# Optimization experiments

Hardware: AMD Instinct MI355X
Metric: run time of the kernel (lower is better)

The kernel has to match this reference:

```python
import jax, jax.numpy as jnp
import numpy as np

OUT_SIZE = 7
SAMPLE_NUM = 2
FEATMAP_STRIDES = (4, 8, 16, 32)
FINEST_SCALE = 56.0
IMG_H, IMG_W = 800, 1216
NUM_ROIS = 1024


def _bilinear_gather(feat, b, ys, xs):
    """Bilinearly sample feat[b] at grid (ys x xs).
    feat: [B,C,H,W]; b: [K] int32; ys,xs: [K,S] float sample coords.
    Returns [K,S,S,C].
    """
    H, W = feat.shape[2], feat.shape[3]
    valid_y = (ys >= -1.0) & (ys <= H)
    valid_x = (xs >= -1.0) & (xs <= W)
    y = jnp.clip(ys, 0.0)
    x = jnp.clip(xs, 0.0)
    yl = jnp.floor(y).astype(jnp.int32)
    xl = jnp.floor(x).astype(jnp.int32)
    # edge handling as in the CUDA roi_align kernel
    y = jnp.where(yl >= H - 1, jnp.asarray(H - 1, y.dtype), y)
    x = jnp.where(xl >= W - 1, jnp.asarray(W - 1, x.dtype), x)
    yl = jnp.minimum(yl, H - 1)
    xl = jnp.minimum(xl, W - 1)
    yh = jnp.minimum(yl + 1, H - 1)
    xh = jnp.minimum(xl + 1, W - 1)
    ly = y - yl.astype(y.dtype)
    lx = x - xl.astype(x.dtype)
    hy = 1.0 - ly
    hx = 1.0 - lx
    bb = b[:, None, None]                      # [K,1,1]
    Yl, Yh = yl[:, :, None], yh[:, :, None]    # [K,S,1]
    Xl, Xh = xl[:, None, :], xh[:, None, :]    # [K,1,S]

    def g(yi, xi):
        return feat[bb, :, yi, xi]             # [K,S,S,C]

    w_ll = (hy[:, :, None] * hx[:, None, :])[..., None]
    w_lh = (hy[:, :, None] * lx[:, None, :])[..., None]
    w_hl = (ly[:, :, None] * hx[:, None, :])[..., None]
    w_hh = (ly[:, :, None] * lx[:, None, :])[..., None]
    out = g(Yl, Xl) * w_ll
    out = out + g(Yl, Xh) * w_lh
    out = out + g(Yh, Xl) * w_hl
    out = out + g(Yh, Xh) * w_hh
    valid = (valid_y[:, :, None] & valid_x[:, None, :])[..., None]
    return jnp.where(valid, out, 0.0)


def roi_align(feat, rois, spatial_scale, out_size=OUT_SIZE, sr=SAMPLE_NUM):
    """RoIAlign (aligned=False, mmdet-v1 style). feat [B,C,H,W], rois [K,5].
    Returns [K,C,out,out].
    """
    K = rois.shape[0]
    C = feat.shape[1]
    b = rois[:, 0].astype(jnp.int32)
    x1 = rois[:, 1] * spatial_scale
    y1 = rois[:, 2] * spatial_scale
    x2 = rois[:, 3] * spatial_scale
    y2 = rois[:, 4] * spatial_scale
    roi_w = jnp.maximum(x2 - x1, 1.0)
    roi_h = jnp.maximum(y2 - y1, 1.0)
    S = out_size * sr
    grid = jnp.arange(S, dtype=feat.dtype) + 0.5  # [S]
    ys = y1[:, None] + grid[None, :] * (roi_h / S)[:, None]  # [K,S]
    xs = x1[:, None] + grid[None, :] * (roi_w / S)[:, None]
    v = _bilinear_gather(feat, b, ys, xs)                    # [K,S,S,C]
    v = v.reshape(K, out_size, sr, out_size, sr, C).mean(axis=(2, 4))
    return jnp.transpose(v, (0, 3, 1, 2))                    # [K,C,out,out]


def setup_inputs() -> dict:
    key = jax.random.key(0)
    ks = jax.random.split(key, 10)
    shapes = [(2, 256, 200, 304), (2, 256, 100, 152), (2, 256, 50, 76), (2, 256, 25, 38)]
    feats = [jax.random.normal(ks[i], s, dtype=jnp.float32) for i, s in enumerate(shapes)]
    K = NUM_ROIS
    b = jax.random.randint(ks[4], (K,), 0, 2).astype(jnp.float32)
    cx = jax.random.uniform(ks[5], (K,)) * IMG_W
    cy = jax.random.uniform(ks[6], (K,)) * IMG_H
    # box sizes spanning 8..512 px so all 4 FPN levels are exercised
    w = 2.0 ** (jax.random.uniform(ks[7], (K,)) * 6.0 + 3.0)
    h = 2.0 ** (jax.random.uniform(ks[8], (K,)) * 6.0 + 3.0)
    x1 = jnp.clip(cx - w * 0.5, 0.0, IMG_W - 1.0)
    y1 = jnp.clip(cy - h * 0.5, 0.0, IMG_H - 1.0)
    x2 = jnp.clip(cx + w * 0.5, 0.0, IMG_W - 1.0)
    y2 = jnp.clip(cy + h * 0.5, 0.0, IMG_H - 1.0)
    x2 = jnp.maximum(x2, x1)
    y2 = jnp.maximum(y2, y1)
    rois = jnp.stack([b, x1, y1, x2, y2], axis=-1)
    return {"feat0": feats[0], "feat1": feats[1], "feat2": feats[2], "feat3": feats[3], "rois": rois}


def reference(feat0, feat1, feat2, feat3, rois):
    feats = [feat0, feat1, feat2, feat3]
    num_levels = len(feats)
    # map_roi_levels
    scale = jnp.sqrt((rois[:, 3] - rois[:, 1] + 1.0) * (rois[:, 4] - rois[:, 2] + 1.0))
    lvls = jnp.floor(jnp.log2(scale / FINEST_SCALE + 1e-6))
    lvls = jnp.clip(lvls, 0, num_levels - 1).astype(jnp.int32)
    out = jnp.zeros((rois.shape[0], feat0.shape[1], OUT_SIZE, OUT_SIZE), dtype=feat0.dtype)
    for i in range(num_levels):
        rf = roi_align(feats[i], rois, 1.0 / FEATMAP_STRIDES[i])
        out = jnp.where((lvls == i)[:, None, None, None], rf, out)
    return out
```

## Files before the change

kernel.cpp:

```cpp
#include <hip/hip_runtime.h>

typedef unsigned int uint32;

namespace {
constexpr int CCH = 256;
constexpr int OUT = 7;
constexpr int S   = 14;
constexpr int NUM_ROIS = 1024;

constexpr int H0 = 200, W0 = 304;
constexpr int H1 = 100, W1 = 152;
constexpr int H2 = 50,  W2 = 76;
constexpr int H3 = 25,  W3 = 38;

constexpr size_t US0 = (size_t)2 * H0 * W0 * CCH;
constexpr size_t US1 = (size_t)2 * H1 * W1 * CCH;
constexpr size_t US2 = (size_t)2 * H2 * W2 * CCH;
constexpr size_t US3 = (size_t)2 * H3 * W3 * CCH;

constexpr int T0 = 10 * H0 * 2;
constexpr int T1 = 5  * H1 * 2;
constexpr int T2 = 3  * H2 * 2;
constexpr int T3 = 2  * H3 * 2;
}

__device__ __forceinline__ unsigned short f2bf(float f) {
    uint32 u = __float_as_uint(f);
    u += 0x7fffu + ((u >> 16) & 1u);
    return (unsigned short)(u >> 16);
}
__device__ __forceinline__ float blo(uint32 u) { return __uint_as_float(u << 16); }
__device__ __forceinline__ float bhi(uint32 u) { return __uint_as_float(u & 0xffff0000u); }

__global__ __launch_bounds__(256) void transpose_bf16(
    const float* __restrict__ f0, const float* __restrict__ f1,
    const float* __restrict__ f2, const float* __restrict__ f3,
    unsigned short* __restrict__ o0, unsigned short* __restrict__ o1,
    unsigned short* __restrict__ o2, unsigned short* __restrict__ o3)
{
    __shared__ __align__(16) unsigned short lds[32 * 264];
    int r = blockIdx.x;
    const float* in; unsigned short* op; int H, W, TX;
    if (r < T0)           {            in = f0; op = o0; H = H0; W = W0; TX = 10; }
    else if (r < T0+T1)   { r -= T0;   in = f1; op = o1; H = H1; W = W1; TX = 5; }
    else if (r < T0+T1+T2){ r -= T0+T1; in = f2; op = o2; H = H2; W = W2; TX = 3; }
    else                  { r -= T0+T1+T2; in = f3; op = o3; H = H3; W = W3; TX = 2; }
    const int tx = r % TX; r /= TX;
    const int y = r % H;
    const int b = r / H;
    const int x0 = tx * 32;
    const int t = threadIdx.x;

    {
        const int xq = t & 7;
        const int c0 = t >> 3;
        const int x  = x0 + 4 * xq;
        const bool w4 = ((W & 3) == 0) && (x + 3 < W);
        #pragma unroll
        for (int i = 0; i < 8; ++i) {
            const int c = c0 + (i << 5);
            const float* src = in + (((size_t)(b * CCH + c) * H + y) * W + x);
            float4 v = make_float4(0.f, 0.f, 0.f, 0.f);
            if (w4) {
                v = *reinterpret_cast<const float4*>(src);
            } else {
                if (x     < W) v.x = src[0];
                if (x + 1 < W) v.y = src[1];
                if (x + 2 < W) v.z = src[2];
                if (x + 3 < W) v.w = src[3];
            }
            unsigned short* dst = &lds[(4 * xq) * 264 + c];
            dst[0 * 264] = f2bf(v.x);
            dst[1 * 264] = f2bf(v.y);
            dst[2 * 264] = f2bf(v.z);
            dst[3 * 264] = f2bf(v.w);
        }
    }
    __syncthreads();
    {
        const int cg  = t & 31;
        const int xr0 = t >> 5;
        #pragma unroll
        for (int i = 0; i < 4; ++i) {
            const int xr = xr0 + 8 * i;
            const int x  = x0 + xr;
            if (x < W) {
                uint4 v = *reinterpret_cast<const uint4*>(&lds[xr * 264 + 8 * cg]);
                *reinterpret_cast<uint4*>(
                    op + (((size_t)b * H + y) * W + x) * CCH + 8 * cg) = v;
            }
        }
    }
}

__global__ __launch_bounds__(256) void roi_gather_bf16(
    const unsigned short* __restrict__ w0, const unsigned short* __restrict__ w1,
    const unsigned short* __restrict__ w2, const unsigned short* __restrict__ w3,
    const float* __restrict__ rois, float* __restrict__ out)
{
    const int k = blockIdx.x;
    const int t = threadIdx.x;

    __shared__ float s_wlo[2][S];
    __shared__ float s_whi[2][S];
    __shared__ int   s_olo[2][S];
    __shared__ int   s_ohi[2][S];
    __shared__ __align__(16) float s_out[25 * 260];

    const float rb  = rois[k*5+0];
    const float rx1 = rois[k*5+1];
    const float ry1 = rois[k*5+2];
    const float rx2 = rois[k*5+3];
    const float ry2 = rois[k*5+4];

    const float sc = sqrtf((rx2 - rx1 + 1.0f) * (ry2 - ry1 + 1.0f));
    int lvl = (int)floorf(log2f(sc * (1.0f/56.0f) + 1e-6f));
    lvl = lvl < 0 ? 0 : (lvl > 3 ? 3 : lvl);

    const unsigned short* fp; int H, W; float sp;
    if (lvl == 0)      { fp = w0; H = H0; W = W0; sp = 0.25f;    }
    else if (lvl == 1) { fp = w1; H = H1; W = W1; sp = 0.125f;   }
    else if (lvl == 2) { fp = w2; H = H2; W = W2; sp = 0.0625f;  }
    else               { fp = w3; H = H3; W = W3; sp = 0.03125f; }

    if (t < 2*S) {
        const int axis = (t >= S) ? 1 : 0;
        const int i = axis ? (t - S) : t;
        const float lo = (axis ? rx1 : ry1) * sp;
        const float hi = (axis ? rx2 : ry2) * sp;
        const int dim  = axis ? W : H;
        const float len = fmaxf(hi - lo, 1.0f);
        const float bin = len * (1.0f / (float)S);
        const float v = lo + ((float)i + 0.5f) * bin;
        const bool valid = (v >= -1.0f) && (v <= (float)dim);
        float vc = fmaxf(v, 0.0f);
        int l = (int)floorf(vc);
        if (l >= dim - 1) { vc = (float)(dim - 1); l = dim - 1; }
        const int h = min(l + 1, dim - 1);
        const float frac = vc - (float)l;
        float wlo = 1.0f - frac;
        float whi = frac;
        if (!valid) { wlo = 0.0f; whi = 0.0f; }
        const int mul = axis ? 64 : W * 64;
        s_wlo[axis][i] = wlo;
        s_whi[axis][i] = whi;
        s_olo[axis][i] = l * mul;
        s_ohi[axis][i] = h * mul;
    }
    __syncthreads();

    const int b = (int)rb;
    const int lane = t & 63;
    const int wv   = t >> 6;
    const uint2* __restrict__ base =
        reinterpret_cast<const uint2*>(fp) + (size_t)b * H * W * 64 + lane;
    float* __restrict__ ob = out + (size_t)k * CCH * (OUT * OUT);

    #pragma unroll
    for (int hf = 0; hf < 2; ++hf) {
        const int bb = hf ? 25 : 0;
        const int ne = hf ? 24 : 25;

        for (int bl = wv; bl < ne; bl += 4) {
            const int bin = bb + bl;
            const int oh = bin / 7;
            const int ow = bin - oh * 7;
            const int sy0 = oh * 2, sx0 = ow * 2;
            float a0 = 0.f, a1 = 0.f, a2 = 0.f, a3 = 0.f;
            #pragma unroll
            for (int dy = 0; dy < 2; ++dy) {
                const float hy = s_wlo[0][sy0 + dy];
                const float ly = s_whi[0][sy0 + dy];
                const int oyl = s_olo[0][sy0 + dy];
                const int oyh = s_ohi[0][sy0 + dy];
                #pragma unroll
                for (int dx = 0; dx < 2; ++dx) {
                    const float hx = s_wlo[1][sx0 + dx];
                    const float lx = s_whi[1][sx0 + dx];
                    const int oxl = s_olo[1][sx0 + dx];
                    const int oxh = s_ohi[1][sx0 + dx];
                    const uint2 qll = base[oyl + oxl];
                    const uint2 qlh = base[oyl + oxh];
                    const uint2 qhl = base[oyh + oxl];
                    const uint2 qhh = base[oyh + oxh];
                    const float wll = hy * hx, wlh = hy * lx;
                    const float whl = ly * hx, whh = ly * lx;
                    a0 += wll*blo(qll.x) + wlh*blo(qlh.x) + whl*blo(qhl.x) + whh*blo(qhh.x);
                    a1 += wll*bhi(qll.x) + wlh*bhi(qlh.x) + whl*bhi(qhl.x) + whh*bhi(qhh.x);
                    a2 += wll*blo(qll.y) + wlh*blo(qlh.y) + whl*blo(qhl.y) + whh*blo(qhh.y);
                    a3 += wll*bhi(qll.y) + wlh*bhi(qlh.y) + whl*bhi(qhl.y) + whh*bhi(qhh.y);
                }
            }
            float4 res = make_float4(a0*0.25f, a1*0.25f, a2*0.25f, a3*0.25f);
            *reinterpret_cast<float4*>(&s_out[bl * 260 + 4 * lane]) = res;
        }
        __syncthreads();

        #pragma unroll 1
        for (int j = 0; j < ne; ++j) {
            const int f = t + j * 256;
            const int c = f / ne;
            const int bl = f - c * ne;
            ob[c * (OUT*OUT) + bb + bl] = s_out[bl * 260 + c];
        }
        __syncthreads();
    }
}

__global__ __launch_bounds__(256) void roi_extract_direct(
    const float* __restrict__ f0, const float* __restrict__ f1,
    const float* __restrict__ f2, const float* __restrict__ f3,
    const float* __restrict__ rois, float* __restrict__ out)
{
    const int k = blockIdx.x;
    const int t = threadIdx.x;

    __shared__ float s_wlo[2][S];
    __shared__ float s_whi[2][S];
    __shared__ int   s_olo[2][S];
    __shared__ int   s_ohi[2][S];

    const float rb  = rois[k*5+0];
    const float rx1 = rois[k*5+1];
    const float ry1 = rois[k*5+2];
    const float rx2 = rois[k*5+3];
    const float ry2 = rois[k*5+4];

    const float sc = sqrtf((rx2 - rx1 + 1.0f) * (ry2 - ry1 + 1.0f));
    int lvl = (int)floorf(log2f(sc * (1.0f/56.0f) + 1e-6f));
    lvl = lvl < 0 ? 0 : (lvl > 3 ? 3 : lvl);

    const float* fp; int H, W; float sp;
    if (lvl == 0)      { fp = f0; H = H0; W = W0; sp = 0.25f;    }
    else if (lvl == 1) { fp = f1; H = H1; W = W1; sp = 0.125f;   }
    else if (lvl == 2) { fp = f2; H = H2; W = W2; sp = 0.0625f;  }
    else               { fp = f3; H = H3; W = W3; sp = 0.03125f; }

    if (t < 2*S) {
        const int axis = (t >= S) ? 1 : 0;
        const int i = axis ? (t - S) : t;
        const float lo = (axis ? rx1 : ry1) * sp;
        const float hi = (axis ? rx2 : ry2) * sp;
        const int dim  = axis ? W : H;
        const float len = fmaxf(hi - lo, 1.0f);
        const float bin = len * (1.0f / (float)S);
        const float v = lo + ((float)i + 0.5f) * bin;
        const bool valid = (v >= -1.0f) && (v <= (float)dim);
        float vc = fmaxf(v, 0.0f);
        int l = (int)floorf(vc);
        if (l >= dim - 1) { vc = (float)(dim - 1); l = dim - 1; }
        const int h = min(l + 1, dim - 1);
        const float frac = vc - (float)l;
        float wlo = 1.0f - frac;
        float whi = frac;
        if (!valid) { wlo = 0.0f; whi = 0.0f; }
        const int mul = axis ? 1 : W;
        s_wlo[axis][i] = wlo;
        s_whi[axis][i] = whi;
        s_olo[axis][i] = l * mul;
        s_ohi[axis][i] = h * mul;
    }
    __syncthreads();

    const int b = (int)rb;
    const float* __restrict__ base = fp + (size_t)(b * CCH + t) * (size_t)(H * W);
    float* __restrict__ obase = out + ((size_t)k * CCH + t) * (OUT * OUT);

    for (int oh = 0; oh < OUT; ++oh) {
        const int sy0 = oh * 2;
        const float hy0 = s_wlo[0][sy0],   ly0 = s_whi[0][sy0];
        const float hy1 = s_wlo[0][sy0+1], ly1 = s_whi[0][sy0+1];
        const int oyl0 = s_olo[0][sy0],   oyh0 = s_ohi[0][sy0];
        const int oyl1 = s_olo[0][sy0+1], oyh1 = s_ohi[0][sy0+1];
        #pragma unroll
        for (int ow = 0; ow < OUT; ++ow) {
            float acc = 0.0f;
            #pragma unroll
            for (int dx = 0; dx < 2; ++dx) {
                const int sx = ow * 2 + dx;
                const float hx = s_wlo[1][sx];
                const float lx = s_whi[1][sx];
                const int oxl = s_olo[1][sx];
                const int oxh = s_ohi[1][sx];
                acc += hy0 * (hx * base[oyl0 + oxl] + lx * base[oyl0 + oxh])
                     + ly0 * (hx * base[oyh0 + oxl] + lx * base[oyh0 + oxh])
                     + hy1 * (hx * base[oyl1 + oxl] + lx * base[oyl1 + oxh])
                     + ly1 * (hx * base[oyh1 + oxl] + lx * base[oyh1 + oxh]);
            }
            obase[oh * OUT + ow] = acc * 0.25f;
        }
    }
}

extern "C" void kernel_launch(void* const* d_in, const int* in_sizes, int n_in,
                              void* d_out, int out_size, void* d_ws, size_t ws_size,
                              hipStream_t stream) {
    const float* f0   = (const float*)d_in[0];
    const float* f1   = (const float*)d_in[1];
    const float* f2   = (const float*)d_in[2];
    const float* f3   = (const float*)d_in[3];
    const float* rois = (const float*)d_in[4];
    float* out = (float*)d_out;

    const size_t need_bytes = (US0 + US1 + US2 + US3) * sizeof(unsigned short);
    if (ws_size >= need_bytes) {
        unsigned short* ws0 = (unsigned short*)d_ws;
        unsigned short* ws1 = ws0 + US0;
        unsigned short* ws2 = ws1 + US1;
        unsigned short* ws3 = ws2 + US2;
        transpose_bf16<<<T0 + T1 + T2 + T3, 256, 0, stream>>>(
            f0, f1, f2, f3, ws0, ws1, ws2, ws3);
        roi_gather_bf16<<<NUM_ROIS, 256, 0, stream>>>(ws0, ws1, ws2, ws3, rois, out);
    } else {
        roi_extract_direct<<<NUM_ROIS, 256, 0, stream>>>(f0, f1, f2, f3, rois, out);
    }
}
```

Measured before the change: 102.1 us.

## Retile NCHW-to-NHWC bf16 transpose over flattened HW with packed channel pairs

Rewrites the feature-map transpose kernel so each block handles 128 flattened spatial positions by 128 channels instead of one row segment of 32 x positions by all 256 channels. Loads are float4 along contiguous HW, two channels are packed into one 32-bit LDS word, and a padded LDS row stride of 70 words is used to cut bank conflicts. Writes become 16-byte stores per 8 channels. The aim is larger contiguous reads, fewer LDS ops and better memory efficiency for the transpose that precedes the ROI gather, at the cost of more registers per thread and partial tiles at level boundaries.

```diff
diff --git a/kernel.cpp b/kernel.cpp
--- a/kernel.cpp
+++ b/kernel.cpp
@@ -13,15 +13,26 @@
 constexpr int H2 = 50,  W2 = 76;
 constexpr int H3 = 25,  W3 = 38;
 
-constexpr size_t US0 = (size_t)2 * H0 * W0 * CCH;
-constexpr size_t US1 = (size_t)2 * H1 * W1 * CCH;
-constexpr size_t US2 = (size_t)2 * H2 * W2 * CCH;
-constexpr size_t US3 = (size_t)2 * H3 * W3 * CCH;
-
-constexpr int T0 = 10 * H0 * 2;
-constexpr int T1 = 5  * H1 * 2;
-constexpr int T2 = 3  * H2 * 2;
-constexpr int T3 = 2  * H3 * 2;
+constexpr int HW0 = H0 * W0;
+constexpr int HW1 = H1 * W1;
+constexpr int HW2 = H2 * W2;
+constexpr int HW3 = H3 * W3;
+
+constexpr size_t US0 = (size_t)2 * HW0 * CCH;
+constexpr size_t US1 = (size_t)2 * HW1 * CCH;
+constexpr size_t US2 = (size_t)2 * HW2 * CCH;
+constexpr size_t US3 = (size_t)2 * HW3 * CCH;
+
+constexpr int TPB0 = (HW0 + 127) / 128;
+constexpr int TPB1 = (HW1 + 127) / 128;
+constexpr int TPB2 = (HW2 + 127) / 128;
+constexpr int TPB3 = (HW3 + 127) / 128;
+constexpr int G0 = 4 * TPB0;
+constexpr int G1 = 4 * TPB1;
+constexpr int G2 = 4 * TPB2;
+constexpr int G3 = 4 * TPB3;
+
+constexpr int LROW = 70;
 }
 
 __device__ __forceinline__ unsigned short f2bf(float f) {
@@ -32,62 +43,88 @@
 __device__ __forceinline__ float blo(uint32 u) { return __uint_as_float(u << 16); }
 __device__ __forceinline__ float bhi(uint32 u) { return __uint_as_float(u & 0xffff0000u); }
 
-__global__ __launch_bounds__(256) void transpose_bf16(
+__global__ __launch_bounds__(256) void transpose_bf16_v3(
     const float* __restrict__ f0, const float* __restrict__ f1,
     const float* __restrict__ f2, const float* __restrict__ f3,
     unsigned short* __restrict__ o0, unsigned short* __restrict__ o1,
     unsigned short* __restrict__ o2, unsigned short* __restrict__ o3)
 {
-    __shared__ __align__(16) unsigned short lds[32 * 264];
+    __shared__ uint32 lds[128 * LROW];
     int r = blockIdx.x;
-    const float* in; unsigned short* op; int H, W, TX;
-    if (r < T0)           {            in = f0; op = o0; H = H0; W = W0; TX = 10; }
-    else if (r < T0+T1)   { r -= T0;   in = f1; op = o1; H = H1; W = W1; TX = 5; }
-    else if (r < T0+T1+T2){ r -= T0+T1; in = f2; op = o2; H = H2; W = W2; TX = 3; }
-    else                  { r -= T0+T1+T2; in = f3; op = o3; H = H3; W = W3; TX = 2; }
-    const int tx = r % TX; r /= TX;
-    const int y = r % H;
-    const int b = r / H;
-    const int x0 = tx * 32;
-    const int t = threadIdx.x;
-
-    {
-        const int xq = t & 7;
-        const int c0 = t >> 3;
-        const int x  = x0 + 4 * xq;
-        const bool w4 = ((W & 3) == 0) && (x + 3 < W);
-        #pragma unroll
-        for (int i = 0; i < 8; ++i) {
-            const int c = c0 + (i << 5);
-            const float* src = in + (((size_t)(b * CCH + c) * H + y) * W + x);
-            float4 v = make_float4(0.f, 0.f, 0.f, 0.f);
-            if (w4) {
-                v = *reinterpret_cast<const float4*>(src);
-            } else {
-                if (x     < W) v.x = src[0];
-                if (x + 1 < W) v.y = src[1];
-                if (x + 2 < W) v.z = src[2];
-                if (x + 3 < W) v.w = src[3];
-            }
-            unsigned short* dst = &lds[(4 * xq) * 264 + c];
-            dst[0 * 264] = f2bf(v.x);
-            dst[1 * 264] = f2bf(v.y);
-            dst[2 * 264] = f2bf(v.z);
-            dst[3 * 264] = f2bf(v.w);
-        }
-    }
-    __syncthreads();
-    {
-        const int cg  = t & 31;
-        const int xr0 = t >> 5;
+    const float* in; unsigned short* op; int HW, TPB;
+    if (r < G0)                {                 in = f0; op = o0; HW = HW0; TPB = TPB0; }
+    else if (r < G0+G1)        { r -= G0;        in = f1; op = o1; HW = HW1; TPB = TPB1; }
+    else if (r < G0+G1+G2)     { r -= G0+G1;     in = f2; op = o2; HW = HW2; TPB = TPB2; }
+    else                       { r -= G0+G1+G2;  in = f3; op = o3; HW = HW3; TPB = TPB3; }
+    const int b    = r / (2 * TPB);
+    int rest = r - b * 2 * TPB;
+    const int half = rest / TPB;
+    const int tile = rest - half * TPB;
+    const int hw0  = tile * 128;
+    const int n    = min(128, HW - hw0);
+    const int t    = threadIdx.x;
+
+    const int hq = t & 15;
+    const int cp = t >> 4;
+
+    const float* src = in + (size_t)(b * CCH + half * 128) * HW + hw0;
+    const bool aligned = ((HW & 3) == 0);
+
+    float4 va[8], vb[8];
+    #pragma unroll
+    for (int h2 = 0; h2 < 2; ++h2) {
         #pragma unroll
         for (int i = 0; i < 4; ++i) {
-            const int xr = xr0 + 8 * i;
-            const int x  = x0 + xr;
-            if (x < W) {
-                uint4 v = *reinterpret_cast<const uint4*>(&lds[xr * 264 + 8 * cg]);
+            const int idx = h2 * 4 + i;
+            const int c   = 2 * (cp + 16 * i);
+            const int hwq = 4 * hq + 64 * h2;
+            const float* p = src + (size_t)c * HW + hwq;
+            const float* q = p + HW;
+            if (aligned && hwq + 3 < n) {
+                va[idx] = *reinterpret_cast<const float4*>(p);
+                vb[idx] = *reinterpret_cast<const float4*>(q);
+            } else {
+                float4 a = make_float4(0.f,0.f,0.f,0.f);
+                float4 bb = make_float4(0.f,0.f,0.f,0.f);
+                if (hwq + 0 < n) { a.x = p[0]; bb.x = q[0]; }
+                if (hwq + 1 < n) { a.y = p[1]; bb.y = q[1]; }
+                if (hwq + 2 < n) { a.z = p[2]; bb.z = q[2]; }
+                if (hwq + 3 < n) { a.w = p[3]; bb.w = q[3]; }
+                va[idx] = a; vb[idx] = bb;
+            }
+        }
+    }
+    #pragma unroll
+    for (int h2 = 0; h2 < 2; ++h2) {
+        #pragma unroll
+        for (int i = 0; i < 4; ++i) {
+            const int idx = h2 * 4 + i;
+            const int col = cp + 16 * i;
+            const int hwr = 4 * hq + 64 * h2;
+            const uint32 u0 = (uint32)f2bf(va[idx].x) | ((uint32)f2bf(vb[idx].x) << 16);
+            const uint32 u1 = (uint32)f2bf(va[idx].y) | ((uint32)f2bf(vb[idx].y) << 16);
+            const uint32 u2 = (uint32)f2bf(va[idx].z) | ((uint32)f2bf(vb[idx].z) << 16);
+            const uint32 u3 = (uint32)f2bf(va[idx].w) | ((uint32)f2bf(vb[idx].w) << 16);
+            lds[(hwr + 0) * LROW + col] = u0;
+            lds[(hwr + 1) * LROW + col] = u1;
+            lds[(hwr + 2) * LROW + col] = u2;
+            lds[(hwr + 3) * LROW + col] = u3;
+        }
+    }
+    __syncthreads();
+
+    {
+        const int cg = t & 15;
+        const int j0 = t >> 4;
+        #pragma unroll
+        for (int it = 0; it < 8; ++it) {
+            const int j = j0 + 16 * it;
+            const uint2 ra = *reinterpret_cast<const uint2*>(&lds[j * LROW + 4 * cg]);
+            const uint2 rb = *reinterpret_cast<const uint2*>(&lds[j * LROW + 4 * cg + 2]);
+            if (j < n) {
+                uint4 v = make_uint4(ra.x, ra.y, rb.x, rb.y);
                 *reinterpret_cast<uint4*>(
-                    op + (((size_t)b * H + y) * W + x) * CCH + 8 * cg) = v;
+                    op + ((size_t)b * HW + hw0 + j) * CCH + half * 128 + 8 * cg) = v;
             }
         }
     }
@@ -308,7 +345,7 @@
         unsigned short* ws1 = ws0 + US0;
         unsigned short* ws2 = ws1 + US1;
         unsigned short* ws3 = ws2 + US2;
-        transpose_bf16<<<T0 + T1 + T2 + T3, 256, 0, stream>>>(
+        transpose_bf16_v3<<<G0 + G1 + G2 + G3, 256, 0, stream>>>(
             f0, f1, f2, f3, ws0, ws1, ws2, ws3);
         roi_gather_bf16<<<NUM_ROIS, 256, 0, stream>>>(ws0, ws1, ws2, ws3, rois, out);
     } else {
```

Result: faster. 90.52 us (-11.4%).

## Rewrite NCHW-to-NHWC bf16 transpose with direct global-to-LDS loads over flattened HW tiles

Applied to the files above, without the earlier changes.

The feature-map transpose now tiles over flattened H*W in 64-element chunks and 128 channels per block, using global_load_lds to move fp32 data straight into LDS without passing through registers. The bf16 conversion moves to the readout phase, where each thread packs 32 channels and writes four 16-byte stores. This aims to raise load bandwidth and cut register and instruction overhead in the transpose, which dominates the pre-pass. In exchange it relies on an AMD-specific intrinsic with an explicit waitcnt, uses a padded LDS stride to limit bank conflicts, and keeps a slower scalar path for unaligned tail tiles.

```diff
diff --git a/kernel.cpp b/kernel.cpp
--- a/kernel.cpp
+++ b/kernel.cpp
@@ -13,15 +13,26 @@
 constexpr int H2 = 50,  W2 = 76;
 constexpr int H3 = 25,  W3 = 38;
 
-constexpr size_t US0 = (size_t)2 * H0 * W0 * CCH;
-constexpr size_t US1 = (size_t)2 * H1 * W1 * CCH;
-constexpr size_t US2 = (size_t)2 * H2 * W2 * CCH;
-constexpr size_t US3 = (size_t)2 * H3 * W3 * CCH;
-
-constexpr int T0 = 10 * H0 * 2;
-constexpr int T1 = 5  * H1 * 2;
-constexpr int T2 = 3  * H2 * 2;
-constexpr int T3 = 2  * H3 * 2;
+constexpr int HW0 = H0 * W0;
+constexpr int HW1 = H1 * W1;
+constexpr int HW2 = H2 * W2;
+constexpr int HW3 = H3 * W3;
+
+constexpr size_t US0 = (size_t)2 * HW0 * CCH;
+constexpr size_t US1 = (size_t)2 * HW1 * CCH;
+constexpr size_t US2 = (size_t)2 * HW2 * CCH;
+constexpr size_t US3 = (size_t)2 * HW3 * CCH;
+
+constexpr int TT0 = (HW0 + 63) / 64;
+constexpr int TT1 = (HW1 + 63) / 64;
+constexpr int TT2 = (HW2 + 63) / 64;
+constexpr int TT3 = (HW3 + 63) / 64;
+constexpr int GG0 = 4 * TT0;
+constexpr int GG1 = 4 * TT1;
+constexpr int GG2 = 4 * TT2;
+constexpr int GG3 = 4 * TT3;
+
+constexpr int RWORDS = 257;
 }
 
 __device__ __forceinline__ unsigned short f2bf(float f) {
@@ -32,64 +43,82 @@
 __device__ __forceinline__ float blo(uint32 u) { return __uint_as_float(u << 16); }
 __device__ __forceinline__ float bhi(uint32 u) { return __uint_as_float(u & 0xffff0000u); }
 
-__global__ __launch_bounds__(256) void transpose_bf16(
+__global__ __launch_bounds__(256) void transpose_gll(
     const float* __restrict__ f0, const float* __restrict__ f1,
     const float* __restrict__ f2, const float* __restrict__ f3,
     unsigned short* __restrict__ o0, unsigned short* __restrict__ o1,
     unsigned short* __restrict__ o2, unsigned short* __restrict__ o3)
 {
-    __shared__ __align__(16) unsigned short lds[32 * 264];
+    __shared__ uint32 lds[32 * RWORDS];
     int r = blockIdx.x;
-    const float* in; unsigned short* op; int H, W, TX;
-    if (r < T0)           {            in = f0; op = o0; H = H0; W = W0; TX = 10; }
-    else if (r < T0+T1)   { r -= T0;   in = f1; op = o1; H = H1; W = W1; TX = 5; }
-    else if (r < T0+T1+T2){ r -= T0+T1; in = f2; op = o2; H = H2; W = W2; TX = 3; }
-    else                  { r -= T0+T1+T2; in = f3; op = o3; H = H3; W = W3; TX = 2; }
-    const int tx = r % TX; r /= TX;
-    const int y = r % H;
-    const int b = r / H;
-    const int x0 = tx * 32;
+    const float* in; unsigned short* op; int HW, TT;
+    if (r < GG0)               {                  in = f0; op = o0; HW = HW0; TT = TT0; }
+    else if (r < GG0+GG1)      { r -= GG0;        in = f1; op = o1; HW = HW1; TT = TT1; }
+    else if (r < GG0+GG1+GG2)  { r -= GG0+GG1;    in = f2; op = o2; HW = HW2; TT = TT2; }
+    else                       { r -= GG0+GG1+GG2; in = f3; op = o3; HW = HW3; TT = TT3; }
+    const int b    = r / (2 * TT);
+    const int rest = r - b * 2 * TT;
+    const int half = rest / TT;
+    const int tile = rest - half * TT;
+    const int hw0  = tile * 64;
+
     const int t = threadIdx.x;
-
-    {
-        const int xq = t & 7;
-        const int c0 = t >> 3;
-        const int x  = x0 + 4 * xq;
-        const bool w4 = ((W & 3) == 0) && (x + 3 < W);
+    const int l = t & 63;
+    const int w = t >> 6;
+
+    const float* src = in + (size_t)(b * CCH + half * 128) * HW;
+    const bool fast = ((HW & 3) == 0) && (hw0 + 64 <= HW);
+
+    if (fast) {
         #pragma unroll
-        for (int i = 0; i < 8; ++i) {
-            const int c = c0 + (i << 5);
-            const float* src = in + (((size_t)(b * CCH + c) * H + y) * W + x);
-            float4 v = make_float4(0.f, 0.f, 0.f, 0.f);
-            if (w4) {
-                v = *reinterpret_cast<const float4*>(src);
-            } else {
-                if (x     < W) v.x = src[0];
-                if (x + 1 < W) v.y = src[1];
-                if (x + 2 < W) v.z = src[2];
-                if (x + 3 < W) v.w = src[3];
+        for (int j = 0; j < 8; ++j) {
+            const int reg = w * 8 + j;
+            const int c   = 4 * reg + (l >> 4);
+            const float* g = src + (size_t)c * HW + hw0 + (l & 15) * 4;
+            __builtin_amdgcn_global_load_lds(
+                (const __attribute__((address_space(1))) void*)g,
+                (__attribute__((address_space(3))) void*)&lds[reg * RWORDS],
+                16, 0, 0);
+        }
+        asm volatile("s_waitcnt vmcnt(0)" ::: "memory");
+        __syncthreads();
+    } else {
+        #pragma unroll 1
+        for (int j = 0; j < 8; ++j) {
+            const int reg = w * 8 + j;
+            const int c   = 4 * reg + (l >> 4);
+            const int hwb = hw0 + (l & 15) * 4;
+            #pragma unroll
+            for (int i = 0; i < 4; ++i) {
+                const int hw = hwb + i;
+                float v = 0.0f;
+                if (hw < HW) v = src[(size_t)c * HW + hw];
+                lds[reg * RWORDS + l * 4 + i] = __float_as_uint(v);
             }
-            unsigned short* dst = &lds[(4 * xq) * 264 + c];
-            dst[0 * 264] = f2bf(v.x);
-            dst[1 * 264] = f2bf(v.y);
-            dst[2 * 264] = f2bf(v.z);
-            dst[3 * 264] = f2bf(v.w);
-        }
-    }
-    __syncthreads();
-    {
-        const int cg  = t & 31;
-        const int xr0 = t >> 5;
+        }
+        __syncthreads();
+    }
+
+    const int n    = min(64, HW - hw0);
+    const int hw   = t >> 2;
+    const int csub = t & 3;
+    if (hw < n) {
+        uint32 outw[16];
         #pragma unroll
-        for (int i = 0; i < 4; ++i) {
-            const int xr = xr0 + 8 * i;
-            const int x  = x0 + xr;
-            if (x < W) {
-                uint4 v = *reinterpret_cast<const uint4*>(&lds[xr * 264 + 8 * cg]);
-                *reinterpret_cast<uint4*>(
-                    op + (((size_t)b * H + y) * W + x) * CCH + 8 * cg) = v;
-            }
-        }
+        for (int m = 0; m < 16; ++m) {
+            const int c0 = csub * 32 + 2 * m;
+            const int c1 = c0 + 1;
+            const uint32 b0 = lds[(c0 >> 2) * RWORDS + (c0 & 3) * 64 + hw];
+            const uint32 b1 = lds[(c1 >> 2) * RWORDS + (c1 & 3) * 64 + hw];
+            outw[m] = (uint32)f2bf(__uint_as_float(b0))
+                    | ((uint32)f2bf(__uint_as_float(b1)) << 16);
+        }
+        unsigned short* ob =
+            op + ((size_t)b * HW + hw0 + hw) * CCH + half * 128 + csub * 32;
+        *reinterpret_cast<uint4*>(ob +  0) = make_uint4(outw[0],  outw[1],  outw[2],  outw[3]);
+        *reinterpret_cast<uint4*>(ob +  8) = make_uint4(outw[4],  outw[5],  outw[6],  outw[7]);
+        *reinterpret_cast<uint4*>(ob + 16) = make_uint4(outw[8],  outw[9],  outw[10], outw[11]);
+        *reinterpret_cast<uint4*>(ob + 24) = make_uint4(outw[12], outw[13], outw[14], outw[15]);
     }
 }
 
@@ -308,7 +337,7 @@
         unsigned short* ws1 = ws0 + US0;
         unsigned short* ws2 = ws1 + US1;
         unsigned short* ws3 = ws2 + US2;
-        transpose_bf16<<<T0 + T1 + T2 + T3, 256, 0, stream>>>(
+        transpose_gll<<<GG0 + GG1 + GG2 + GG3, 256, 0, stream>>>(
             f0, f1, f2, f3, ws0, ws1, ws2, ws3);
         roi_gather_bf16<<<NUM_ROIS, 256, 0, stream>>>(ws0, ws1, ws2, ws3, rois, out);
     } else {
```

Measured after the change: 98.88 us, median of 2. 3.2% less time.

## Retile NCHW-to-NHWC bf16 transpose over flattened spatial tiles of 512 by 64 channels

Applied to the files above, without the earlier changes.

Replaces the per-row, 32-pixel transpose tiles with tiles of 512 flattened spatial positions by 64 channels. Each thread reads long contiguous float4 runs from two channels, packs channel pairs into 32-bit bf16 words in a padded LDS tile, and writes 16-byte NHWC chunks. The aim is longer, better-coalesced reads, fewer blocks and wider LDS accesses for this memory-bound layout conversion. In exchange it uses a larger LDS footprint (about 64 KB per block), which can lower occupancy, and adds a slow scalar path for partial tiles.

```diff
diff --git a/kernel.cpp b/kernel.cpp
--- a/kernel.cpp
+++ b/kernel.cpp
@@ -13,15 +13,26 @@
 constexpr int H2 = 50,  W2 = 76;
 constexpr int H3 = 25,  W3 = 38;
 
-constexpr size_t US0 = (size_t)2 * H0 * W0 * CCH;
-constexpr size_t US1 = (size_t)2 * H1 * W1 * CCH;
-constexpr size_t US2 = (size_t)2 * H2 * W2 * CCH;
-constexpr size_t US3 = (size_t)2 * H3 * W3 * CCH;
-
-constexpr int T0 = 10 * H0 * 2;
-constexpr int T1 = 5  * H1 * 2;
-constexpr int T2 = 3  * H2 * 2;
-constexpr int T3 = 2  * H3 * 2;
+constexpr int HW0 = H0 * W0;
+constexpr int HW1 = H1 * W1;
+constexpr int HW2 = H2 * W2;
+constexpr int HW3 = H3 * W3;
+
+constexpr size_t US0 = (size_t)2 * HW0 * CCH;
+constexpr size_t US1 = (size_t)2 * HW1 * CCH;
+constexpr size_t US2 = (size_t)2 * HW2 * CCH;
+constexpr size_t US3 = (size_t)2 * HW3 * CCH;
+
+constexpr int NT0 = (HW0 + 511) / 512;
+constexpr int NT1 = (HW1 + 511) / 512;
+constexpr int NT2 = (HW2 + 511) / 512;
+constexpr int NT3 = (HW3 + 511) / 512;
+constexpr int GQ0 = 8 * NT0;
+constexpr int GQ1 = 8 * NT1;
+constexpr int GQ2 = 8 * NT2;
+constexpr int GQ3 = 8 * NT3;
+
+constexpr int LPAD = 516;
 }
 
 __device__ __forceinline__ unsigned short f2bf(float f) {
@@ -29,65 +40,87 @@
     u += 0x7fffu + ((u >> 16) & 1u);
     return (unsigned short)(u >> 16);
 }
+__device__ __forceinline__ uint32 pk(float a, float b) {
+    return (uint32)f2bf(a) | ((uint32)f2bf(b) << 16);
+}
 __device__ __forceinline__ float blo(uint32 u) { return __uint_as_float(u << 16); }
 __device__ __forceinline__ float bhi(uint32 u) { return __uint_as_float(u & 0xffff0000u); }
 
-__global__ __launch_bounds__(256) void transpose_bf16(
+__global__ __launch_bounds__(256) void transpose_seq(
     const float* __restrict__ f0, const float* __restrict__ f1,
     const float* __restrict__ f2, const float* __restrict__ f3,
     unsigned short* __restrict__ o0, unsigned short* __restrict__ o1,
     unsigned short* __restrict__ o2, unsigned short* __restrict__ o3)
 {
-    __shared__ __align__(16) unsigned short lds[32 * 264];
+    __shared__ uint32 lds[32 * LPAD];
     int r = blockIdx.x;
-    const float* in; unsigned short* op; int H, W, TX;
-    if (r < T0)           {            in = f0; op = o0; H = H0; W = W0; TX = 10; }
-    else if (r < T0+T1)   { r -= T0;   in = f1; op = o1; H = H1; W = W1; TX = 5; }
-    else if (r < T0+T1+T2){ r -= T0+T1; in = f2; op = o2; H = H2; W = W2; TX = 3; }
-    else                  { r -= T0+T1+T2; in = f3; op = o3; H = H3; W = W3; TX = 2; }
-    const int tx = r % TX; r /= TX;
-    const int y = r % H;
-    const int b = r / H;
-    const int x0 = tx * 32;
+    const float* in; unsigned short* op; int HW, NT;
+    if (r < GQ0)                {                   in = f0; op = o0; HW = HW0; NT = NT0; }
+    else if (r < GQ0+GQ1)       { r -= GQ0;         in = f1; op = o1; HW = HW1; NT = NT1; }
+    else if (r < GQ0+GQ1+GQ2)   { r -= GQ0+GQ1;     in = f2; op = o2; HW = HW2; NT = NT2; }
+    else                        { r -= GQ0+GQ1+GQ2; in = f3; op = o3; HW = HW3; NT = NT3; }
+    const int b    = r / (4 * NT);
+    const int rem  = r - b * 4 * NT;
+    const int q    = rem / NT;
+    const int tile = rem - q * NT;
+    const int hw0  = tile * 512;
+
     const int t = threadIdx.x;
+    const int l = t & 63;
+    const int w = t >> 6;
+
+    const float* src = in + (size_t)(b * CCH + q * 64) * HW;
+    const bool fast = ((HW & 3) == 0) && (hw0 + 512 <= HW);
+
+    if (fast) {
+        #pragma unroll
+        for (int p = 0; p < 8; ++p) {
+            const int cp = w * 8 + p;
+            const float* pa = src + (size_t)(2 * cp) * HW + hw0;
+            const float* pb = pa + HW;
+            const float4 A0 = *reinterpret_cast<const float4*>(pa + 4 * l);
+            const float4 A1 = *reinterpret_cast<const float4*>(pa + 256 + 4 * l);
+            const float4 B0 = *reinterpret_cast<const float4*>(pb + 4 * l);
+            const float4 B1 = *reinterpret_cast<const float4*>(pb + 256 + 4 * l);
+            uint32* d = &lds[cp * LPAD + 4 * l];
+            *reinterpret_cast<uint4*>(d) =
+                make_uint4(pk(A0.x, B0.x), pk(A0.y, B0.y), pk(A0.z, B0.z), pk(A0.w, B0.w));
+            *reinterpret_cast<uint4*>(d + 256) =
+                make_uint4(pk(A1.x, B1.x), pk(A1.y, B1.y), pk(A1.z, B1.z), pk(A1.w, B1.w));
+        }
+    } else {
+        #pragma unroll 1
+        for (int p = 0; p < 8; ++p) {
+            const int cp = w * 8 + p;
+            const float* pa = src + (size_t)(2 * cp) * HW;
+            const float* pb = pa + HW;
+            #pragma unroll 1
+            for (int k = 0; k < 8; ++k) {
+                const int idx = 64 * k + l;
+                const int hw = hw0 + idx;
+                float a = 0.0f, bb = 0.0f;
+                if (hw < HW) { a = pa[hw]; bb = pb[hw]; }
+                lds[cp * LPAD + idx] = pk(a, bb);
+            }
+        }
+    }
+    __syncthreads();
 
     {
-        const int xq = t & 7;
-        const int c0 = t >> 3;
-        const int x  = x0 + 4 * xq;
-        const bool w4 = ((W & 3) == 0) && (x + 3 < W);
+        const int n  = min(512, HW - hw0);
+        const int sc = t & 7;
+        const int r0 = t >> 3;
         #pragma unroll
-        for (int i = 0; i < 8; ++i) {
-            const int c = c0 + (i << 5);
-            const float* src = in + (((size_t)(b * CCH + c) * H + y) * W + x);
-            float4 v = make_float4(0.f, 0.f, 0.f, 0.f);
-            if (w4) {
-                v = *reinterpret_cast<const float4*>(src);
-            } else {
-                if (x     < W) v.x = src[0];
-                if (x + 1 < W) v.y = src[1];
-                if (x + 2 < W) v.z = src[2];
-                if (x + 3 < W) v.w = src[3];
-            }
-            unsigned short* dst = &lds[(4 * xq) * 264 + c];
-            dst[0 * 264] = f2bf(v.x);
-            dst[1 * 264] = f2bf(v.y);
-            dst[2 * 264] = f2bf(v.z);
-            dst[3 * 264] = f2bf(v.w);
-        }
-    }
-    __syncthreads();
-    {
-        const int cg  = t & 31;
-        const int xr0 = t >> 5;
-        #pragma unroll
-        for (int i = 0; i < 4; ++i) {
-            const int xr = xr0 + 8 * i;
-            const int x  = x0 + xr;
-            if (x < W) {
-                uint4 v = *reinterpret_cast<const uint4*>(&lds[xr * 264 + 8 * cg]);
+        for (int k = 0; k < 16; ++k) {
+            const int row = r0 + 32 * k;
+            const uint32 v0 = lds[(4 * sc + 0) * LPAD + row];
+            const uint32 v1 = lds[(4 * sc + 1) * LPAD + row];
+            const uint32 v2 = lds[(4 * sc + 2) * LPAD + row];
+            const uint32 v3 = lds[(4 * sc + 3) * LPAD + row];
+            if (row < n) {
                 *reinterpret_cast<uint4*>(
-                    op + (((size_t)b * H + y) * W + x) * CCH + 8 * cg) = v;
+                    op + ((size_t)b * HW + hw0 + row) * CCH + q * 64 + 8 * sc) =
+                    make_uint4(v0, v1, v2, v3);
             }
         }
     }
@@ -308,7 +341,7 @@
         unsigned short* ws1 = ws0 + US0;
         unsigned short* ws2 = ws1 + US1;
         unsigned short* ws3 = ws2 + US2;
-        transpose_bf16<<<T0 + T1 + T2 + T3, 256, 0, stream>>>(
+        transpose_seq<<<GQ0 + GQ1 + GQ2 + GQ3, 256, 0, stream>>>(
             f0, f1, f2, f3, ws0, ws1, ws2, ws3);
         roi_gather_bf16<<<NUM_ROIS, 256, 0, stream>>>(ws0, ws1, ws2, ws3, rois, out);
     } else {
```

Result: slower. 112.0 us (+9.7%).
